# Kernel optimization log

Hardware: AMD Instinct MI355X
Metric: run time of the kernel (lower is better)

The kernel has to match this reference:

```python
import jax, jax.numpy as jnp
import numpy as np

# Production-scale dims (see shape_source)
B, H, W, C = 8, 64, 64, 256
KH, KW = 3, 3
BASES = 16
FILTERS = 256


def setup_inputs() -> dict:
    key = jax.random.key(0)
    k1, k2, k3, k4 = jax.random.split(key, 4)
    x = jax.random.normal(k1, (B, H, W, C), dtype=jnp.float32)
    # P: channel-mixing matrix [C, C] (initialized to identity in build, then assigned)
    P = jax.random.normal(k2, (C, C), dtype=jnp.float32) * 0.05
    # Q: per-channel basis kernels [C, kh, kw, bases]
    Q = jax.random.normal(k3, (C, KH, KW, BASES), dtype=jnp.float32) * 0.1
    # S: basis-combination weights [C, bases, filters]
    S = jax.random.normal(k4, (C, BASES, FILTERS), dtype=jnp.float32) * 0.05
    return {"x": x, "P": P, "Q": Q, "S": S}


def reference(x, P, Q, S):
    # --- Step 1: channel mixing (the vectorized_map over calculate_J) ---
    # J[o] = sum_c x[..., c] * P[o, c]  ->  one GEMM over channels
    mixed = jnp.einsum('bhwc,oc->bhwo', x, P)  # [B,H,W,C]

    C_ = P.shape[0]
    kh, kw, bases = Q.shape[1], Q.shape[2], Q.shape[3]

    # --- Step 2: per-channel conv with `bases` basis kernels (the map_fn loop) ---
    # Expressed as ONE grouped (depthwise-style) conv: group c produces outputs
    # [c*bases : (c+1)*bases], matching kernel flatten order (c, b).
    rhs = jnp.transpose(Q, (1, 2, 0, 3)).reshape(kh, kw, 1, C_ * bases)  # HWIO
    dw = jax.lax.conv_general_dilated(
        mixed, rhs, window_strides=(1, 1), padding='VALID',
        dimension_numbers=('NHWC', 'HWIO', 'NHWC'),
        feature_group_count=C_,
    )  # [B, H-kh+1, W-kw+1, C*bases], channel index k = c*bases + b

    b, h, w, _ = dw.shape
    # tau in the original: [B, h, w, bases, C]
    tau = dw.reshape(b, h, w, C_, bases).transpose(0, 1, 2, 4, 3)

    # --- Step 3: basis-weighted combination (the vectorized_map over calculate_O) ---
    # Original flattens tau row-major over (bases, C) and S[:, :, f] row-major over
    # (C, bases), then does an elementwise dot over the flat axis. Replicate exactly.
    Tflat = tau.reshape(b, h, w, bases * C_)          # flat index k = b_idx*C + c
    Sflat = S.reshape(C_ * bases, S.shape[-1])        # flat index k = c*bases + b_idx
    O = jnp.einsum('bhwk,kf->bhwf', Tflat, Sflat)     # [B, h, w, filters]
    return O
```

## Files before the change

### kernel.cpp

```cpp
#include <hip/hip_runtime.h>
#include <hip/hip_bf16.h>

typedef __attribute__((ext_vector_type(4))) float f32x4;
typedef __attribute__((ext_vector_type(8))) short bf16x8;

#define M_TOT 30752

__device__ __forceinline__ unsigned short f2bf(float f) {
  unsigned int u = __float_as_uint(f);
  u = u + 0x7FFF + ((u >> 16) & 1);
  return (unsigned short)(u >> 16);
}

__device__ __forceinline__ void gload16(const void* g, void* l) {
  __builtin_amdgcn_global_load_lds((const __attribute__((address_space(1))) unsigned int*)g,
                                   (__attribute__((address_space(3))) unsigned int*)l,
                                   16, 0, 0);
}

__global__ void cast_x(const float* __restrict__ x, unsigned short* __restrict__ xb) {
  int i = blockIdx.x * 256 + threadIdx.x;
  const f32x4* xp = (const f32x4*)x;
  f32x4 a = xp[2 * i];
  f32x4 b = xp[2 * i + 1];
  bf16x8 o;
  o[0] = (short)f2bf(a[0]); o[1] = (short)f2bf(a[1]);
  o[2] = (short)f2bf(a[2]); o[3] = (short)f2bf(a[3]);
  o[4] = (short)f2bf(b[0]); o[5] = (short)f2bf(b[1]);
  o[6] = (short)f2bf(b[2]); o[7] = (short)f2bf(b[3]);
  ((bf16x8*)xb)[i] = o;
}

__global__ void keff_k(const float* __restrict__ Q, const float* __restrict__ S,
                       float* __restrict__ Keff) {
  int bid = blockIdx.x;
  int o = bid / 9;
  int kk = bid - o * 9;
  int f = threadIdx.x;
  int qb = o * 144 + kk * 16;
  int sb = ((o >> 4) * 16 + (o & 15)) * 256 + f;
  float acc = 0.f;
#pragma unroll
  for (int bi = 0; bi < 16; ++bi)
    acc = fmaf(Q[qb + bi], S[sb + bi * 65536], acc);
  Keff[bid * 256 + f] = acc;
}

__global__ void k2t_k(const float* __restrict__ P, const float* __restrict__ Keff,
                      unsigned short* __restrict__ K2t) {
  int kk = blockIdx.x >> 4;
  int f0 = (blockIdx.x & 15) * 16;
  int ci = threadIdx.x;
  float acc[16];
#pragma unroll
  for (int j = 0; j < 16; ++j) acc[j] = 0.f;
  for (int o = 0; o < 256; ++o) {
    float pv = P[o * 256 + ci];
    const float* ke = Keff + (o * 9 + kk) * 256 + f0;
#pragma unroll
    for (int j = 0; j < 16; ++j) acc[j] = fmaf(pv, ke[j], acc[j]);
  }
#pragma unroll
  for (int j = 0; j < 16; ++j)
    K2t[kk * 65536 + (f0 + j) * 256 + ci] = f2bf(acc[j]);
}

__global__ __launch_bounds__(512) void conv_gemm(const unsigned short* __restrict__ xb,
                                                 const unsigned short* __restrict__ K2t,
                                                 float* __restrict__ out) {
  __shared__ unsigned short A0[128 * 64];
  __shared__ unsigned short A1[128 * 64];
  __shared__ unsigned short A2[128 * 64];
  __shared__ unsigned short B0[256 * 64];
  __shared__ unsigned short B1[256 * 64];
  __shared__ unsigned short B2[256 * 64];

  const int tid = threadIdx.x;
  const int lane = tid & 63;
  const int wm = (tid >> 6) >> 2;
  const int wn = (tid >> 6) & 3;
  const int m0 = blockIdx.x * 128;

  const int swslot = ((tid & 7) ^ ((tid >> 3) & 7)) * 8;
  const int rA = tid >> 3;

  int gA0, gA1;
  {
    int m = m0 + rA; if (m >= M_TOT) m = M_TOT - 1;
    int b = m / 3844; int rem = m - b * 3844;
    int h = rem / 62; int w = rem - h * 62;
    gA0 = ((b * 64 + h) * 64 + w) * 256 + swslot;
    m = m0 + rA + 64; if (m >= M_TOT) m = M_TOT - 1;
    b = m / 3844; rem = m - b * 3844;
    h = rem / 62; w = rem - h * 62;
    gA1 = ((b * 64 + h) * 64 + w) * 256 + swslot;
  }

  f32x4 zero = {0.f, 0.f, 0.f, 0.f};
  f32x4 acc[4][4];
#pragma unroll
  for (int i = 0; i < 4; ++i)
#pragma unroll
    for (int j = 0; j < 4; ++j) acc[i][j] = zero;

  const int rl = lane & 15;
  const int kg = lane >> 4;
  const int xm = (lane & 7) << 4;

#define STAGE(t, bufA, bufB)                                                   \
  {                                                                            \
    int kk_ = (t) >> 2, cb_ = (t) & 3;                                         \
    int kh_ = kk_ / 3, kw_ = kk_ - kh_ * 3;                                    \
    int offA_ = kh_ * 16384 + kw_ * 256 + cb_ * 64;                            \
    int offB_ = kk_ * 65536 + cb_ * 64 + swslot;                               \
    gload16(xb + gA0 + offA_, &bufA[tid * 8]);                                 \
    gload16(xb + gA1 + offA_, &bufA[(tid + 512) * 8]);                         \
    _Pragma("unroll")                                                          \
    for (int q = 0; q < 4; ++q)                                                \
      gload16(K2t + offB_ + (rA + 64 * q) * 256, &bufB[(tid + 512 * q) * 8]);  \
  }

#define WAIT_BAR(t)                                                            \
  {                                                                            \
    if ((t) == 35) asm volatile("s_waitcnt vmcnt(0)" ::: "memory");            \
    else           asm volatile("s_waitcnt vmcnt(6)" ::: "memory");            \
    __builtin_amdgcn_sched_barrier(0);                                         \
    __builtin_amdgcn_s_barrier();                                              \
    __builtin_amdgcn_sched_barrier(0);                                         \
  }

#define COMPUTE(t, bufA, bufB)                                                 \
  {                                                                            \
    bf16x8 af[4][2], bfr[4][2];                                                \
    _Pragma("unroll")                                                          \
    for (int mi = 0; mi < 4; ++mi) {                                           \
      int rb = (wm * 64 + mi * 16 + rl) * 128;                                 \
      _Pragma("unroll")                                                        \
      for (int ks = 0; ks < 2; ++ks) {                                         \
        int cbyte = (ks * 64 + kg * 16) ^ xm;                                  \
        af[mi][ks] = *(const bf16x8*)((const char*)bufA + rb + cbyte);         \
      }                                                                        \
    }                                                                          \
    _Pragma("unroll")                                                          \
    for (int ni = 0; ni < 4; ++ni) {                                           \
      int rb = (wn * 64 + ni * 16 + rl) * 128;                                 \
      _Pragma("unroll")                                                        \
      for (int ks = 0; ks < 2; ++ks) {                                         \
        int cbyte = (ks * 64 + kg * 16) ^ xm;                                  \
        bfr[ni][ks] = *(const bf16x8*)((const char*)bufB + rb + cbyte);        \
      }                                                                        \
    }                                                                          \
    _Pragma("unroll")                                                          \
    for (int ks = 0; ks < 2; ++ks)                                             \
      _Pragma("unroll")                                                        \
      for (int mi = 0; mi < 4; ++mi)                                           \
        _Pragma("unroll")                                                      \
        for (int ni = 0; ni < 4; ++ni)                                         \
          acc[mi][ni] = __builtin_amdgcn_mfma_f32_16x16x32_bf16(               \
              af[mi][ks], bfr[ni][ks], acc[mi][ni], 0, 0, 0);                  \
  }

  STAGE(0, A0, B0);
  STAGE(1, A1, B1);

  for (int tt = 0; tt < 12; ++tt) {
    int t0 = tt * 3;
    WAIT_BAR(t0);
    if (t0 + 2 < 36) STAGE(t0 + 2, A2, B2);
    __builtin_amdgcn_sched_barrier(0);
    COMPUTE(t0, A0, B0);

    WAIT_BAR(t0 + 1);
    if (t0 + 3 < 36) STAGE(t0 + 3, A0, B0);
    __builtin_amdgcn_sched_barrier(0);
    COMPUTE(t0 + 1, A1, B1);

    WAIT_BAR(t0 + 2);
    if (t0 + 4 < 36) STAGE(t0 + 4, A1, B1);
    __builtin_amdgcn_sched_barrier(0);
    COMPUTE(t0 + 2, A2, B2);
  }

#pragma unroll
  for (int mi = 0; mi < 4; ++mi) {
    int mb = m0 + wm * 64 + mi * 16 + kg * 4;
#pragma unroll
    for (int ni = 0; ni < 4; ++ni) {
      int f = wn * 64 + ni * 16 + rl;
#pragma unroll
      for (int r = 0; r < 4; ++r) {
        int m = mb + r;
        if (m < M_TOT) out[m * 256 + f] = acc[mi][ni][r];
      }
    }
  }
#undef STAGE
#undef WAIT_BAR
#undef COMPUTE
}

extern "C" void kernel_launch(void* const* d_in, const int* in_sizes, int n_in,
                              void* d_out, int out_size, void* d_ws, size_t ws_size,
                              hipStream_t stream) {
  const float* x = (const float*)d_in[0];
  const float* P = (const float*)d_in[1];
  const float* Q = (const float*)d_in[2];
  const float* S = (const float*)d_in[3];
  float* out = (float*)d_out;

  char* ws = (char*)d_ws;
  unsigned short* xb   = (unsigned short*)ws;
  float*          Keff = (float*)(ws + 16777216);
  unsigned short* K2t  = (unsigned short*)(ws + 16777216 + 2359296);

  cast_x<<<4096, 256, 0, stream>>>(x, xb);
  keff_k<<<2304, 256, 0, stream>>>(Q, S, Keff);
  k2t_k<<<144, 256, 0, stream>>>(P, Keff, K2t);
  conv_gemm<<<241, 512, 0, stream>>>(xb, K2t, out);
}
```

Measured before the change: 87.33 us.

## Fuse prep kernels into one launch and split GEMM stages into k-phases

Merges the x cast, the Keff computation and the P*Keff weight fold into a single prep kernel. Keff is now built in LDS per block, so its global round trip goes away and two launches are removed. The conv GEMM main loop now splits each 64-wide K tile into two half-phases. A and B global loads are interleaved with LDS reads, and an extra barrier plus s_setprio are added around the MFMA clusters. The extra barrier per stage and the recomputed Keff across the 32 f-blocks per kk are the costs paid for this.

Result: slower. 95.54 us (+9.4%).

```diff
diff --git a/kernel.cpp b/kernel.cpp
--- a/kernel.cpp
+++ b/kernel.cpp
@@ -18,51 +18,79 @@
                                    16, 0, 0);
 }
 
-__global__ void cast_x(const float* __restrict__ x, unsigned short* __restrict__ xb) {
-  int i = blockIdx.x * 256 + threadIdx.x;
-  const f32x4* xp = (const f32x4*)x;
-  f32x4 a = xp[2 * i];
-  f32x4 b = xp[2 * i + 1];
-  bf16x8 o;
-  o[0] = (short)f2bf(a[0]); o[1] = (short)f2bf(a[1]);
-  o[2] = (short)f2bf(a[2]); o[3] = (short)f2bf(a[3]);
-  o[4] = (short)f2bf(b[0]); o[5] = (short)f2bf(b[1]);
-  o[6] = (short)f2bf(b[2]); o[7] = (short)f2bf(b[3]);
-  ((bf16x8*)xb)[i] = o;
-}
-
-__global__ void keff_k(const float* __restrict__ Q, const float* __restrict__ S,
-                       float* __restrict__ Keff) {
-  int bid = blockIdx.x;
-  int o = bid / 9;
-  int kk = bid - o * 9;
-  int f = threadIdx.x;
-  int qb = o * 144 + kk * 16;
-  int sb = ((o >> 4) * 16 + (o & 15)) * 256 + f;
-  float acc = 0.f;
-#pragma unroll
-  for (int bi = 0; bi < 16; ++bi)
-    acc = fmaf(Q[qb + bi], S[sb + bi * 65536], acc);
-  Keff[bid * 256 + f] = acc;
-}
-
-__global__ void k2t_k(const float* __restrict__ P, const float* __restrict__ Keff,
-                      unsigned short* __restrict__ K2t) {
-  int kk = blockIdx.x >> 4;
-  int f0 = (blockIdx.x & 15) * 16;
-  int ci = threadIdx.x;
-  float acc[16];
-#pragma unroll
-  for (int j = 0; j < 16; ++j) acc[j] = 0.f;
-  for (int o = 0; o < 256; ++o) {
-    float pv = P[o * 256 + ci];
-    const float* ke = Keff + (o * 9 + kk) * 256 + f0;
-#pragma unroll
-    for (int j = 0; j < 16; ++j) acc[j] = fmaf(pv, ke[j], acc[j]);
-  }
-#pragma unroll
-  for (int j = 0; j < 16; ++j)
-    K2t[kk * 65536 + (f0 + j) * 256 + ci] = f2bf(acc[j]);
+__global__ __launch_bounds__(256) void prep_k(const float* __restrict__ x,
+                                              const float* __restrict__ P,
+                                              const float* __restrict__ Q,
+                                              const float* __restrict__ S,
+                                              unsigned short* __restrict__ xb,
+                                              unsigned short* __restrict__ K2t) {
+  __shared__ float ldsQ[256 * 16];
+  __shared__ float ldsK[256 * 8];
+
+  const int bid = blockIdx.x;
+  const int t = threadIdx.x;
+
+  if (bid < 4096) {
+    int i = bid * 256 + t;
+    const f32x4* xp = (const f32x4*)x;
+    f32x4 a = xp[2 * i];
+    f32x4 b = xp[2 * i + 1];
+    bf16x8 o;
+    o[0] = (short)f2bf(a[0]); o[1] = (short)f2bf(a[1]);
+    o[2] = (short)f2bf(a[2]); o[3] = (short)f2bf(a[3]);
+    o[4] = (short)f2bf(b[0]); o[5] = (short)f2bf(b[1]);
+    o[6] = (short)f2bf(b[2]); o[7] = (short)f2bf(b[3]);
+    ((bf16x8*)xb)[i] = o;
+    return;
+  }
+
+  const int bid2 = bid - 4096;
+  const int kk = bid2 >> 5;
+  const int f0 = (bid2 & 31) * 8;
+
+  {
+    const f32x4* qp = (const f32x4*)(Q + t * 144 + kk * 16);
+    f32x4* lq = (f32x4*)(ldsQ + t * 16);
+    lq[0] = qp[0]; lq[1] = qp[1]; lq[2] = qp[2]; lq[3] = qp[3];
+  }
+  __syncthreads();
+
+  {
+    int o = t;
+    const float* sp = S + (o >> 4) * 4096 + (o & 15) * 256 + f0;
+    float ka[8];
+#pragma unroll
+    for (int j = 0; j < 8; ++j) ka[j] = 0.f;
+#pragma unroll
+    for (int bi = 0; bi < 16; ++bi) {
+      const f32x4* s4 = (const f32x4*)(sp + bi * 65536);
+      f32x4 sa = s4[0], sb = s4[1];
+      float qv = ldsQ[o * 16 + bi];
+      ka[0] = fmaf(qv, sa[0], ka[0]); ka[1] = fmaf(qv, sa[1], ka[1]);
+      ka[2] = fmaf(qv, sa[2], ka[2]); ka[3] = fmaf(qv, sa[3], ka[3]);
+      ka[4] = fmaf(qv, sb[0], ka[4]); ka[5] = fmaf(qv, sb[1], ka[5]);
+      ka[6] = fmaf(qv, sb[2], ka[6]); ka[7] = fmaf(qv, sb[3], ka[7]);
+    }
+#pragma unroll
+    for (int j = 0; j < 8; ++j) ldsK[o * 8 + j] = ka[j];
+  }
+  __syncthreads();
+
+  {
+    int ci = t;
+    float acc[8];
+#pragma unroll
+    for (int j = 0; j < 8; ++j) acc[j] = 0.f;
+#pragma unroll 4
+    for (int o = 0; o < 256; ++o) {
+      float pv = P[o * 256 + ci];
+#pragma unroll
+      for (int j = 0; j < 8; ++j) acc[j] = fmaf(pv, ldsK[o * 8 + j], acc[j]);
+    }
+#pragma unroll
+    for (int j = 0; j < 8; ++j)
+      K2t[kk * 65536 + (f0 + j) * 256 + ci] = f2bf(acc[j]);
+  }
 }
 
 __global__ __launch_bounds__(512) void conv_gemm(const unsigned short* __restrict__ xb,
@@ -107,78 +135,69 @@
   const int kg = lane >> 4;
   const int xm = (lane & 7) << 4;
 
-#define STAGE(t, bufA, bufB)                                                   \
+#define STAGE_A(t, bufA)                                                       \
   {                                                                            \
     int kk_ = (t) >> 2, cb_ = (t) & 3;                                         \
     int kh_ = kk_ / 3, kw_ = kk_ - kh_ * 3;                                    \
     int offA_ = kh_ * 16384 + kw_ * 256 + cb_ * 64;                            \
-    int offB_ = kk_ * 65536 + cb_ * 64 + swslot;                               \
     gload16(xb + gA0 + offA_, &bufA[tid * 8]);                                 \
     gload16(xb + gA1 + offA_, &bufA[(tid + 512) * 8]);                         \
+  }
+
+#define STAGE_B(t, bufB)                                                       \
+  {                                                                            \
+    int kk_ = (t) >> 2, cb_ = (t) & 3;                                         \
+    int offB_ = kk_ * 65536 + cb_ * 64 + swslot;                               \
     _Pragma("unroll")                                                          \
     for (int q = 0; q < 4; ++q)                                                \
       gload16(K2t + offB_ + (rA + 64 * q) * 256, &bufB[(tid + 512 * q) * 8]);  \
   }
 
-#define WAIT_BAR(t)                                                            \
+#define PHASE(ks, bufA, bufB, STAGE_STMT)                                      \
+  {                                                                            \
+    bf16x8 af[4], bfr[4];                                                      \
+    int cbyte = ((ks) * 64 + kg * 16) ^ xm;                                    \
+    _Pragma("unroll")                                                          \
+    for (int mi = 0; mi < 4; ++mi)                                             \
+      af[mi] = *(const bf16x8*)((const char*)bufA + (wm * 64 + mi * 16 + rl) * 128 + cbyte); \
+    _Pragma("unroll")                                                          \
+    for (int ni = 0; ni < 4; ++ni)                                             \
+      bfr[ni] = *(const bf16x8*)((const char*)bufB + (wn * 64 + ni * 16 + rl) * 128 + cbyte); \
+    STAGE_STMT;                                                                \
+    asm volatile("s_waitcnt lgkmcnt(0)" ::: "memory");                         \
+    __builtin_amdgcn_sched_barrier(0);                                         \
+    __builtin_amdgcn_s_setprio(1);                                             \
+    _Pragma("unroll")                                                          \
+    for (int mi = 0; mi < 4; ++mi)                                             \
+      _Pragma("unroll")                                                        \
+      for (int ni = 0; ni < 4; ++ni)                                           \
+        acc[mi][ni] = __builtin_amdgcn_mfma_f32_16x16x32_bf16(                 \
+            af[mi], bfr[ni], acc[mi][ni], 0, 0, 0);                            \
+    __builtin_amdgcn_s_setprio(0);                                             \
+  }
+
+#define STEP(t, cA, cB, nA, nB)                                                \
   {                                                                            \
     if ((t) == 35) asm volatile("s_waitcnt vmcnt(0)" ::: "memory");            \
     else           asm volatile("s_waitcnt vmcnt(6)" ::: "memory");            \
     __builtin_amdgcn_sched_barrier(0);                                         \
     __builtin_amdgcn_s_barrier();                                              \
     __builtin_amdgcn_sched_barrier(0);                                         \
-  }
-
-#define COMPUTE(t, bufA, bufB)                                                 \
-  {                                                                            \
-    bf16x8 af[4][2], bfr[4][2];                                                \
-    _Pragma("unroll")                                                          \
-    for (int mi = 0; mi < 4; ++mi) {                                           \
-      int rb = (wm * 64 + mi * 16 + rl) * 128;                                 \
-      _Pragma("unroll")                                                        \
-      for (int ks = 0; ks < 2; ++ks) {                                         \
-        int cbyte = (ks * 64 + kg * 16) ^ xm;                                  \
-        af[mi][ks] = *(const bf16x8*)((const char*)bufA + rb + cbyte);         \
-      }                                                                        \
-    }                                                                          \
-    _Pragma("unroll")                                                          \
-    for (int ni = 0; ni < 4; ++ni) {                                           \
-      int rb = (wn * 64 + ni * 16 + rl) * 128;                                 \
-      _Pragma("unroll")                                                        \
-      for (int ks = 0; ks < 2; ++ks) {                                         \
-        int cbyte = (ks * 64 + kg * 16) ^ xm;                                  \
-        bfr[ni][ks] = *(const bf16x8*)((const char*)bufB + rb + cbyte);        \
-      }                                                                        \
-    }                                                                          \
-    _Pragma("unroll")                                                          \
-    for (int ks = 0; ks < 2; ++ks)                                             \
-      _Pragma("unroll")                                                        \
-      for (int mi = 0; mi < 4; ++mi)                                           \
-        _Pragma("unroll")                                                      \
-        for (int ni = 0; ni < 4; ++ni)                                         \
-          acc[mi][ni] = __builtin_amdgcn_mfma_f32_16x16x32_bf16(               \
-              af[mi][ks], bfr[ni][ks], acc[mi][ni], 0, 0, 0);                  \
-  }
-
-  STAGE(0, A0, B0);
-  STAGE(1, A1, B1);
+    PHASE(0, cA, cB, { if ((t) + 2 < 36) STAGE_A((t) + 2, nA); })              \
+    __builtin_amdgcn_sched_barrier(0);                                         \
+    __builtin_amdgcn_s_barrier();                                              \
+    __builtin_amdgcn_sched_barrier(0);                                         \
+    PHASE(1, cA, cB, { if ((t) + 2 < 36) STAGE_B((t) + 2, nB); })              \
+  }
+
+  STAGE_A(0, A0); STAGE_B(0, B0);
+  STAGE_A(1, A1); STAGE_B(1, B1);
 
   for (int tt = 0; tt < 12; ++tt) {
     int t0 = tt * 3;
-    WAIT_BAR(t0);
-    if (t0 + 2 < 36) STAGE(t0 + 2, A2, B2);
-    __builtin_amdgcn_sched_barrier(0);
-    COMPUTE(t0, A0, B0);
-
-    WAIT_BAR(t0 + 1);
-    if (t0 + 3 < 36) STAGE(t0 + 3, A0, B0);
-    __builtin_amdgcn_sched_barrier(0);
-    COMPUTE(t0 + 1, A1, B1);
-
-    WAIT_BAR(t0 + 2);
-    if (t0 + 4 < 36) STAGE(t0 + 4, A1, B1);
-    __builtin_amdgcn_sched_barrier(0);
-    COMPUTE(t0 + 2, A2, B2);
+    STEP(t0,     A0, B0, A2, B2);
+    STEP(t0 + 1, A1, B1, A0, B0);
+    STEP(t0 + 2, A2, B2, A1, B1);
   }
 
 #pragma unroll
@@ -194,9 +213,10 @@
       }
     }
   }
-#undef STAGE
-#undef WAIT_BAR
-#undef COMPUTE
+#undef STAGE_A
+#undef STAGE_B
+#undef PHASE
+#undef STEP
 }
 
 extern "C" void kernel_launch(void* const* d_in, const int* in_sizes, int n_in,
@@ -209,12 +229,9 @@
   float* out = (float*)d_out;
 
   char* ws = (char*)d_ws;
-  unsigned short* xb   = (unsigned short*)ws;
-  float*          Keff = (float*)(ws + 16777216);
-  unsigned short* K2t  = (unsigned short*)(ws + 16777216 + 2359296);
-
-  cast_x<<<4096, 256, 0, stream>>>(x, xb);
-  keff_k<<<2304, 256, 0, stream>>>(Q, S, Keff);
-  k2t_k<<<144, 256, 0, stream>>>(P, Keff, K2t);
+  unsigned short* xb  = (unsigned short*)ws;
+  unsigned short* K2t = (unsigned short*)(ws + 16777216);
+
+  prep_k<<<4096 + 288, 256, 0, stream>>>(x, P, Q, S, xb, K2t);
   conv_gemm<<<241, 512, 0, stream>>>(xb, K2t, out);
 }
```
